# Kernel optimization log

Measured on AMD Instinct MI355X. Metric: run time of the kernel, lower is better.

## Reference

```python
import jax, jax.numpy as jnp
import numpy as np

B, C, N = 4, 512, 4096
CQK = C // 8


def setup_inputs() -> dict:
    key = jax.random.key(0)
    ks = jax.random.split(key, 8)
    return {
        "minibatch": jax.random.normal(ks[0], (B, C, N), dtype=jnp.float32),
        "Wq": jax.random.normal(ks[1], (CQK, C), dtype=jnp.float32) * 0.02,
        "bq": jax.random.normal(ks[2], (CQK,), dtype=jnp.float32) * 0.02,
        "Wk": jax.random.normal(ks[3], (CQK, C), dtype=jnp.float32) * 0.02,
        "bk": jax.random.normal(ks[4], (CQK,), dtype=jnp.float32) * 0.02,
        "Wv": jax.random.normal(ks[5], (C, C), dtype=jnp.float32) * 0.02,
        "bv": jax.random.normal(ks[6], (C,), dtype=jnp.float32) * 0.02,
        "gamma": jax.random.normal(ks[7], (1,), dtype=jnp.float32),
    }


def reference(minibatch, Wq, bq, Wk, bk, Wv, bv, gamma):
    # 1x1 Conv1d == per-position channel matmul. minibatch: [B, C, N]
    q = jnp.einsum('dc,bcn->bdn', Wq, minibatch) + bq[None, :, None]  # [B, C/8, N]
    k = jnp.einsum('dc,bcn->bdn', Wk, minibatch) + bk[None, :, None]  # [B, C/8, N]
    v = jnp.einsum('dc,bcn->bdn', Wv, minibatch) + bv[None, :, None]  # [B, C, N]
    # logits[b,i,j] = q_i . k_j  (note: original computes a triu mask but never uses it)
    logits = jnp.einsum('bdn,bdm->bnm', q, k)  # [B, N, N]
    probs = jax.nn.softmax(logits, axis=-1)
    # read[b,c,i] = sum_j v[b,c,j] * probs[b,i,j]
    read = jnp.einsum('bcm,bnm->bcn', v, probs)  # [B, C, N]
    return gamma[0] * read + minibatch
```

## Files before the change

kernel.cpp:

```cpp
#include <hip/hip_runtime.h>
#include <stdint.h>

typedef unsigned short u16;
typedef unsigned int u32;
typedef __attribute__((ext_vector_type(8))) short short8;
typedef __attribute__((ext_vector_type(4))) short s16x4;
typedef __attribute__((ext_vector_type(4))) float f32x4;
typedef __attribute__((ext_vector_type(16))) float f32x16;
typedef __attribute__((ext_vector_type(4))) int int4v;

#define MFMA16(a,b,c) __builtin_amdgcn_mfma_f32_16x16x32_bf16(a,b,c,0,0,0)
#define MFMA32(a,b,c) __builtin_amdgcn_mfma_f32_32x32x16_bf16(a,b,c,0,0,0)

constexpr int B_ = 4, C_ = 512, N_ = 4096, D_ = 64;

static __device__ __forceinline__ u16 f2bf(float f) {
    uint32_t u = __builtin_bit_cast(uint32_t, f);
    uint32_t r = (u + 0x7FFFu + ((u >> 16) & 1u)) >> 16;
    return (u16)r;
}

static __device__ __forceinline__ void gload_lds16(const void* g, void* l) {
    __builtin_amdgcn_global_load_lds(
        (const __attribute__((address_space(1))) u32*)g,
        (__attribute__((address_space(3))) u32*)l, 16, 0, 0);
}

__global__ __launch_bounds__(256) void prep_and_transpose(
        const float* __restrict__ x, u16* __restrict__ xT,
        const float* __restrict__ Wq, const float* __restrict__ bq,
        const float* __restrict__ Wk, const float* __restrict__ bk,
        const float* __restrict__ Wv, const float* __restrict__ bv,
        u16* __restrict__ Wcat, float* __restrict__ biascat) {
    const float LOG2E = 1.44269504088896340736f;
    if (blockIdx.z == B_) {
        int base = (blockIdx.y * 64 + blockIdx.x) * 256 + threadIdx.x;
        for (int idx = base; idx < 640 * 512; idx += 64 * 8 * 256) {
            int row = idx >> 9, col = idx & 511;
            float w;
            if (row < 64)        w = Wq[row * 512 + col] * LOG2E;
            else if (row < 128)  w = Wk[(row - 64) * 512 + col];
            else                 w = Wv[(row - 128) * 512 + col];
            Wcat[idx] = f2bf(w);
        }
        if (base < 640) {
            float bb;
            if (base < 64)       bb = bq[base] * LOG2E;
            else if (base < 128) bb = bk[base - 64];
            else                 bb = bv[base - 128];
            biascat[base] = bb;
        }
        return;
    }
    __shared__ float tile[64][65];
    int n0 = blockIdx.x * 64, c0 = blockIdx.y * 64, b = blockIdx.z;
    int t = threadIdx.x;
    int colq = (t & 15) * 4, rowb = t >> 4;
    const float* xb = x + (size_t)b * C_ * N_;
#pragma unroll
    for (int k = 0; k < 4; k++) {
        int row = rowb + 16 * k;
        float4 xv = *reinterpret_cast<const float4*>(&xb[(size_t)(c0 + row) * N_ + n0 + colq]);
        tile[row][colq + 0] = xv.x;
        tile[row][colq + 1] = xv.y;
        tile[row][colq + 2] = xv.z;
        tile[row][colq + 3] = xv.w;
    }
    __syncthreads();
    u16* xTb = xT + (size_t)b * N_ * C_;
#pragma unroll
    for (int k = 0; k < 4; k++) {
        int n = rowb + 16 * k;
        ushort4 o;
        o.x = f2bf(tile[colq + 0][n]);
        o.y = f2bf(tile[colq + 1][n]);
        o.z = f2bf(tile[colq + 2][n]);
        o.w = f2bf(tile[colq + 3][n]);
        *reinterpret_cast<ushort4*>(&xTb[(size_t)(n0 + n) * C_ + c0 + colq]) = o;
    }
}

__global__ __launch_bounds__(256) void proj_gemm(const u16* __restrict__ Wcat,
                                                 const float* __restrict__ biascat,
                                                 const u16* __restrict__ xT,
                                                 u16* __restrict__ qT, u16* __restrict__ kT,
                                                 u16* __restrict__ v) {
    int wg = blockIdx.x;
    int xcd = wg & 7, slot = wg >> 3;
    int b = xcd >> 1;
    int m0 = (slot >> 3) * 64;
    int n0 = ((xcd & 1) * 8 + (slot & 7)) * 256;
    int wave = threadIdx.x >> 6, lane = threadIdx.x & 63;
    n0 += wave * 64;
    int lr = lane & 15, lc = lane >> 4;
    const u16* xTb = xT + (size_t)b * N_ * C_;

    f32x4 acc[4][4] = {};
    short8 aF[4], bF[4], aFn[4], bFn[4];
#pragma unroll
    for (int ma = 0; ma < 4; ma++)
        aF[ma] = *reinterpret_cast<const short8*>(&Wcat[(size_t)(m0 + ma * 16 + lr) * 512 + lc * 8]);
#pragma unroll
    for (int na = 0; na < 4; na++)
        bF[na] = *reinterpret_cast<const short8*>(&xTb[(size_t)(n0 + na * 16 + lr) * 512 + lc * 8]);

    for (int k0 = 0; k0 < 512; k0 += 32) {
        if (k0 < 480) {
            int kn = k0 + 32;
#pragma unroll
            for (int ma = 0; ma < 4; ma++)
                aFn[ma] = *reinterpret_cast<const short8*>(&Wcat[(size_t)(m0 + ma * 16 + lr) * 512 + kn + lc * 8]);
#pragma unroll
            for (int na = 0; na < 4; na++)
                bFn[na] = *reinterpret_cast<const short8*>(&xTb[(size_t)(n0 + na * 16 + lr) * 512 + kn + lc * 8]);
        }
#pragma unroll
        for (int ma = 0; ma < 4; ma++)
#pragma unroll
            for (int na = 0; na < 4; na++)
                acc[ma][na] = MFMA16(aF[ma], bF[na], acc[ma][na]);
#pragma unroll
        for (int t = 0; t < 4; t++) { aF[t] = aFn[t]; bF[t] = bFn[t]; }
    }
#pragma unroll
    for (int ma = 0; ma < 4; ma++) {
#pragma unroll
        for (int r = 0; r < 4; r++) {
            int m = m0 + ma * 16 + lc * 4 + r;
            float bias = biascat[m];
#pragma unroll
            for (int na = 0; na < 4; na++) {
                int n = n0 + na * 16 + lr;
                u16 hv = f2bf(acc[ma][na][r] + bias);
                if (m < 64)
                    qT[((size_t)b * N_ + n) * D_ + m] = hv;
                else if (m < 128)
                    kT[((size_t)b * N_ + n) * D_ + (m - 64)] = hv;
                else {
                    int nl = n & 15;
                    int np = (nl & 3) | ((nl & 4) << 1) | ((nl & 8) >> 1);
                    v[((size_t)b * C_ + (m - 128)) * (size_t)N_ + (n & ~15) + np] = hv;
                }
            }
        }
    }
}

__global__ __launch_bounds__(512, 2) void attn(const u16* __restrict__ qT, const u16* __restrict__ kT,
                                               const u16* __restrict__ v, const float* __restrict__ x,
                                               const float* __restrict__ gamma_p, float* __restrict__ out) {
    int blk = blockIdx.x;
    int xcd = blk & 7, rest = blk >> 3;
    int b = xcd >> 1;
    int cs = (xcd & 1) + 2 * (rest & 1);
    int itile = rest >> 1;
    int c0 = cs * 128;
    int ib0 = itile * 256;

    int tid = threadIdx.x;
    int wv = tid >> 6, lane = tid & 63;
    int li = lane & 31, hi = lane >> 5;

    __shared__ char smem[98304];

    const u16* qTb = qT + (size_t)b * N_ * D_;
    const u16* kTb = kT + (size_t)b * N_ * D_;
    const u16* vb  = v  + (size_t)b * C_ * N_;

    short8 qf[4];
#pragma unroll
    for (int dc = 0; dc < 4; dc++)
        qf[dc] = *reinterpret_cast<const short8*>(
            &qTb[(size_t)(ib0 + wv * 32 + li) * D_ + dc * 16 + hi * 8]);

    f32x16 acc[4] = {};
    float lsum = 0.f;

    auto STAGE = [&](int t, int buf) {
        int jb = t * 128;
        char* Kb = smem + buf * 49152;
        char* Vb = Kb + 16384;
#pragma unroll
        for (int q = 0; q < 2; q++) {
            int ki = 2 * wv + q;
            int p = ki >> 1, jh2 = ki & 1;
            gload_lds16(kTb + (size_t)(jb + jh2 * 64 + lane) * D_ + p * 8,
                        Kb + p * 2048 + jh2 * 1024);
        }
#pragma unroll
        for (int q = 0; q < 4; q++) {
            int vi = 4 * wv + q;
            int qp = vi >> 1, ch = vi & 1;
            int j16b = qp >> 1, hb = qp & 1;
            gload_lds16(vb + (size_t)(c0 + ch * 64 + lane) * N_ + jb + j16b * 16 + hb * 8,
                        Vb + qp * 2048 + ch * 1024);
        }
    };

    STAGE(0, 0);
    asm volatile("s_waitcnt vmcnt(0)" ::: "memory");
    __builtin_amdgcn_s_barrier();
    asm volatile("" ::: "memory");

    for (int t = 0; t < 32; t++) {
        int buf = t & 1;
        char* Kb = smem + buf * 49152;
        char* Vb = Kb + 16384;

        if (t < 31) STAGE(t + 1, buf ^ 1);

        auto S_PHASE = [&](int jc, short8* PAo) {
            short8 kf0 = *reinterpret_cast<const short8*>(Kb + (0 + hi) * 2048 + (jc * 32 + li) * 16);
            short8 kf1 = *reinterpret_cast<const short8*>(Kb + (2 + hi) * 2048 + (jc * 32 + li) * 16);
            short8 kf2 = *reinterpret_cast<const short8*>(Kb + (4 + hi) * 2048 + (jc * 32 + li) * 16);
            short8 kf3 = *reinterpret_cast<const short8*>(Kb + (6 + hi) * 2048 + (jc * 32 + li) * 16);
            f32x16 S = {};
            S = MFMA32(kf0, qf[0], S);
            S = MFMA32(kf1, qf[1], S);
            S = MFMA32(kf2, qf[2], S);
            S = MFMA32(kf3, qf[3], S);
            float p[16];
#pragma unroll
            for (int r = 0; r < 16; r++) p[r] = __builtin_amdgcn_exp2f(S[r]);
            lsum += (((p[0]+p[1])+(p[2]+p[3]))+((p[4]+p[5])+(p[6]+p[7])))
                  + (((p[8]+p[9])+(p[10]+p[11]))+((p[12]+p[13])+(p[14]+p[15])));
            u32 w[8];
#pragma unroll
            for (int k = 0; k < 8; k++)
                asm("v_cvt_pk_bf16_f32 %0, %1, %2" : "=v"(w[k]) : "v"(p[2 * k]), "v"(p[2 * k + 1]));
            int4v a0 = { (int)w[0], (int)w[1], (int)w[2], (int)w[3] };
            int4v a1 = { (int)w[4], (int)w[5], (int)w[6], (int)w[7] };
            PAo[0] = __builtin_bit_cast(short8, a0);
            PAo[1] = __builtin_bit_cast(short8, a1);
        };
        auto PV_PHASE = [&](int jc, const short8* PAi) {
#pragma unroll
            for (int ct = 0; ct < 4; ct++) {
                short8 vf0 = *reinterpret_cast<const short8*>(
                    Vb + ((jc * 2 + 0) * 2 + hi) * 2048 + (ct * 32 + li) * 16);
                short8 vf1 = *reinterpret_cast<const short8*>(
                    Vb + ((jc * 2 + 1) * 2 + hi) * 2048 + (ct * 32 + li) * 16);
                acc[ct] = MFMA32(PAi[0], vf0, acc[ct]);
                acc[ct] = MFMA32(PAi[1], vf1, acc[ct]);
            }
        };

        short8 PA_A[2], PA_B[2];
        S_PHASE(0, PA_A);
        S_PHASE(1, PA_B);
        PV_PHASE(0, PA_A);
        S_PHASE(2, PA_A);
        PV_PHASE(1, PA_B);
        S_PHASE(3, PA_B);
        PV_PHASE(2, PA_A);
        PV_PHASE(3, PA_B);

        asm volatile("s_waitcnt vmcnt(0)" ::: "memory");
        __builtin_amdgcn_s_barrier();
        asm volatile("" ::: "memory");
    }

    float lfull = lsum + __shfl_xor(lsum, 32);
    float g = gamma_p[0];
    float* olds = reinterpret_cast<float*>(smem + wv * 4608);
    const float* xb = x + (size_t)b * C_ * N_;
    float* ob = out + (size_t)b * C_ * N_;
#pragma unroll
    for (int ct = 0; ct < 4; ct++) {
#pragma unroll
        for (int r = 0; r < 16; r++) {
            int crow = (r & 3) + 8 * (r >> 2) + 4 * hi;
            float linv = 1.0f / __shfl(lfull, crow);
            olds[li * 36 + crow] = g * acc[ct][r] * linv;
        }
        asm volatile("s_waitcnt lgkmcnt(0)" ::: "memory");
#pragma unroll
        for (int cp = 0; cp < 4; cp++) {
            int c_l = cp * 8 + (lane >> 3);
            int i4 = (lane & 7) * 4;
            float4 o4 = *reinterpret_cast<const float4*>(&olds[c_l * 36 + i4]);
            size_t off = (size_t)(c0 + ct * 32 + c_l) * N_ + ib0 + wv * 32 + i4;
            float4 xv = *reinterpret_cast<const float4*>(&xb[off]);
            float4 ov = { o4.x + xv.x, o4.y + xv.y, o4.z + xv.z, o4.w + xv.w };
            *reinterpret_cast<float4*>(&ob[off]) = ov;
        }
        asm volatile("s_waitcnt lgkmcnt(0)" ::: "memory");
    }
}

extern "C" void kernel_launch(void* const* d_in, const int* in_sizes, int n_in,
                              void* d_out, int out_size, void* d_ws, size_t ws_size,
                              hipStream_t stream) {
    const float* x     = (const float*)d_in[0];
    const float* Wq    = (const float*)d_in[1];
    const float* bq    = (const float*)d_in[2];
    const float* Wk    = (const float*)d_in[3];
    const float* bk    = (const float*)d_in[4];
    const float* Wv    = (const float*)d_in[5];
    const float* bv    = (const float*)d_in[6];
    const float* gamma = (const float*)d_in[7];
    float* out = (float*)d_out;

    char* ws = (char*)d_ws;
    u16*   xT      = (u16*)ws;
    u16*   Wcat    = (u16*)(ws + (size_t)16777216);
    float* biascat = (float*)(ws + (size_t)16777216 + 655360);
    u16*   qT      = (u16*)(ws + (size_t)16777216 + 655360 + 4096);
    u16*   kT      = qT + (size_t)B_ * N_ * D_;
    u16*   v       = kT + (size_t)B_ * N_ * D_;

    prep_and_transpose<<<dim3(N_ / 64, C_ / 64, B_ + 1), 256, 0, stream>>>(
        x, xT, Wq, bq, Wk, bk, Wv, bv, Wcat, biascat);
    proj_gemm<<<640, 256, 0, stream>>>(Wcat, biascat, xT, qT, kT, v);
    attn<<<256, 512, 0, stream>>>(qT, kT, v, x, gamma, out);
}
```

Measured before the change: 169.1 us.

## Stage projection GEMM operands through double-buffered LDS with 128x128 block tiles

Reworks the projection GEMM so each workgroup computes a 128x128 tile, with its four waves arranged 2x2. A and B slices are staged into double-buffered shared memory via global_load_lds, replacing per-wave direct global register loads. This lets waves share operand loads instead of each fetching its own A fragment. The cost is a barrier and vmcnt wait every k-step, and the grid mapping changes to match the new tile shape.

Result: faster. 140.3 us (-17.0%).

```diff
diff --git a/kernel.cpp b/kernel.cpp
--- a/kernel.cpp
+++ b/kernel.cpp
@@ -88,49 +88,68 @@
     int wg = blockIdx.x;
     int xcd = wg & 7, slot = wg >> 3;
     int b = xcd >> 1;
-    int m0 = (slot >> 3) * 64;
-    int n0 = ((xcd & 1) * 8 + (slot & 7)) * 256;
+    int m0 = (slot >> 4) * 128;
+    int n0 = ((xcd & 1) * 16 + (slot & 15)) * 128;
     int wave = threadIdx.x >> 6, lane = threadIdx.x & 63;
-    n0 += wave * 64;
     int lr = lane & 15, lc = lane >> 4;
+    int wm = (wave & 1) * 64, wn = (wave >> 1) * 64;
     const u16* xTb = xT + (size_t)b * N_ * C_;
 
+    __shared__ u16 Ab[2][128 * 32];
+    __shared__ u16 Bb[2][128 * 32];
+
+    auto STAGE = [&](int ks, int buf) {
+        int k0 = ks * 32;
+        int row = lane >> 2, co = (lane & 3) * 8;
+#pragma unroll
+        for (int q = 0; q < 2; q++) {
+            int ch = 2 * wave + q;
+            gload_lds16(&Wcat[(size_t)(m0 + ch * 16 + row) * 512 + k0 + co],
+                        (char*)Ab[buf] + ch * 1024);
+            gload_lds16(&xTb[(size_t)(n0 + ch * 16 + row) * 512 + k0 + co],
+                        (char*)Bb[buf] + ch * 1024);
+        }
+    };
+
     f32x4 acc[4][4] = {};
-    short8 aF[4], bF[4], aFn[4], bFn[4];
-#pragma unroll
-    for (int ma = 0; ma < 4; ma++)
-        aF[ma] = *reinterpret_cast<const short8*>(&Wcat[(size_t)(m0 + ma * 16 + lr) * 512 + lc * 8]);
-#pragma unroll
-    for (int na = 0; na < 4; na++)
-        bF[na] = *reinterpret_cast<const short8*>(&xTb[(size_t)(n0 + na * 16 + lr) * 512 + lc * 8]);
-
-    for (int k0 = 0; k0 < 512; k0 += 32) {
-        if (k0 < 480) {
-            int kn = k0 + 32;
-#pragma unroll
-            for (int ma = 0; ma < 4; ma++)
-                aFn[ma] = *reinterpret_cast<const short8*>(&Wcat[(size_t)(m0 + ma * 16 + lr) * 512 + kn + lc * 8]);
-#pragma unroll
-            for (int na = 0; na < 4; na++)
-                bFn[na] = *reinterpret_cast<const short8*>(&xTb[(size_t)(n0 + na * 16 + lr) * 512 + kn + lc * 8]);
+
+    STAGE(0, 0);
+    asm volatile("s_waitcnt vmcnt(0)" ::: "memory");
+    __builtin_amdgcn_s_barrier();
+    asm volatile("" ::: "memory");
+
+    for (int ks = 0; ks < 16; ks++) {
+        int buf = ks & 1;
+        if (ks < 15) STAGE(ks + 1, buf ^ 1);
+
+        short8 aF[4], bF[4];
+#pragma unroll
+        for (int t = 0; t < 4; t++) {
+            aF[t] = *reinterpret_cast<const short8*>(
+                (const char*)Ab[buf] + (wm + t * 16 + lr) * 64 + lc * 16);
+            bF[t] = *reinterpret_cast<const short8*>(
+                (const char*)Bb[buf] + (wn + t * 16 + lr) * 64 + lc * 16);
         }
 #pragma unroll
         for (int ma = 0; ma < 4; ma++)
 #pragma unroll
             for (int na = 0; na < 4; na++)
                 acc[ma][na] = MFMA16(aF[ma], bF[na], acc[ma][na]);
-#pragma unroll
-        for (int t = 0; t < 4; t++) { aF[t] = aFn[t]; bF[t] = bFn[t]; }
-    }
+
+        asm volatile("s_waitcnt vmcnt(0)" ::: "memory");
+        __builtin_amdgcn_s_barrier();
+        asm volatile("" ::: "memory");
+    }
+
 #pragma unroll
     for (int ma = 0; ma < 4; ma++) {
 #pragma unroll
         for (int r = 0; r < 4; r++) {
-            int m = m0 + ma * 16 + lc * 4 + r;
+            int m = m0 + wm + ma * 16 + lc * 4 + r;
             float bias = biascat[m];
 #pragma unroll
             for (int na = 0; na < 4; na++) {
-                int n = n0 + na * 16 + lr;
+                int n = n0 + wn + na * 16 + lr;
                 u16 hv = f2bf(acc[ma][na][r] + bias);
                 if (m < 64)
                     qT[((size_t)b * N_ + n) * D_ + m] = hv;
```
